# Kernel optimization log

Measured on AMD Instinct MI355X. Metric: run time of the kernel, lower is better.

The kernel has to match this reference:

```python
import jax, jax.numpy as jnp
import numpy as np

RHO = 1.0
L = 50
RS = np.array([20, 40, 80, 160], dtype=np.int32)

def _get_index():
    S = []
    for m in range(-L // 2, L // 2 + 1):
        for n in range(-L // 2, L // 2 + 1):
            if abs(m * n) <= RHO * L // 2:
                S.append((m, n))
    return np.array(S, dtype=np.int32)

IDX = _get_index()          # [449, 2] (m, n) pairs
K = IDX.shape[0]            # 449
B, N, M = 8, 65536, 2       # batch, sequence length, Nmodes (dual-pol)


def setup_inputs() -> dict:
    key = jax.random.key(0)
    ks = jax.random.split(key, 8)
    shp = (B, N, M)
    inp = {
        "E_real": jax.random.normal(ks[0], shp, jnp.float32),
        "E_imag": jax.random.normal(ks[1], shp, jnp.float32),
        "F_real": jax.random.normal(ks[2], shp, jnp.float32),
        "F_imag": jax.random.normal(ks[3], shp, jnp.float32),
        "C1_real": jax.random.normal(ks[4], (len(RS), K), jnp.float32) * 0.01,
        "C1_imag": jax.random.normal(ks[5], (len(RS), K), jnp.float32) * 0.01,
        "C2_real": jax.random.normal(ks[6], (len(RS), K), jnp.float32) * 0.01,
        "C2_imag": jax.random.normal(ks[7], (len(RS), K), jnp.float32) * 0.01,
    }
    # task_info columns: (P [dBm], Fi, Fs [Hz], Nch); Fs must be 2e9 * some Rs entry
    ti = np.zeros((B, 4), dtype=np.float32)
    ti[:, 0] = 2.0
    ti[:, 2] = RS[np.arange(B) % len(RS)].astype(np.float32) * 2e9
    inp["task_info"] = jnp.asarray(ti)
    return inp


def _forward(E_real, E_imag, F_real, F_imag, C1_real, C1_imag, C2_real, C2_imag, task_info):
    E = E_real + 1j * E_imag    # [B, N, M] complex64
    F = F_real + 1j * F_imag

    # choose_C: map Fs -> row of C tables (sorted-Rs order, as in the torch code)
    rs_sorted = jnp.sort(jnp.asarray(RS))
    x = (task_info[:, 2] / 2e9).astype(jnp.int32)              # [B]
    ind = jnp.argmax(x[:, None] == rs_sorted[None, :], axis=-1)  # [B]
    C1 = (C1_real + 1j * C1_imag)[ind]                         # [B, K]
    C2 = (C2_real + 1j * C2_imag)[ind]                         # [B, K]

    ms = jnp.asarray(IDX[:, 0])
    ns = jnp.asarray(IDX[:, 1])

    def step(acc, xs):
        m, n, c1, c2 = xs                                       # c1, c2: [B]
        En  = jnp.roll(E, n, axis=-2)
        Em  = jnp.roll(E, m, axis=-2)
        Emn = jnp.roll(E, m + n, axis=-2)
        Fn  = jnp.roll(F, n, axis=-2)
        Fmn = jnp.roll(F, m + n, axis=-2)
        A = En * jnp.conj(Fmn) * c1[:, None, None] + Fn * jnp.conj(Emn) * c2[:, None, None]
        # (A + A.roll(1, dim=-1)) swaps/combines the two polarizations
        return acc + (A + jnp.roll(A, 1, axis=-1)) * Em, None

    acc, _ = jax.lax.scan(step, jnp.zeros_like(E), (ms, ns, C1.T, C2.T))

    P = jnp.power(10.0, task_info[:, 0] / 10.0) / E.shape[-1]   # [B]
    Eo = F + (jnp.sqrt(P) ** 3)[:, None, None] * acc
    return E[:, L:-L, :], Eo[:, L:-L, :]


def reference(E_real, E_imag, F_real, F_imag, C1_real, C1_imag, C2_real, C2_imag, task_info):
    return _forward(E_real, E_imag, F_real, F_imag,
                    C1_real, C1_imag, C2_real, C2_imag, task_info)
```

## Files before the change

### kernel.cpp

```cpp
#include <hip/hip_runtime.h>
#include <hip/hip_bf16.h>


namespace {

constexpr int NSEQ    = 65536;
constexpr int BATCH   = 8;
constexpr int KTAPS   = 449;
constexpr int NM      = 25;
constexpr int THREADS = 256;
constexpr int TILE    = 512;
constexpr int WIN     = TILE + 4 * NM;
constexpr int GHW     = TILE + 2 * NM;

typedef float v2f __attribute__((ext_vector_type(2)));

__device__ inline v2f pkfma(float s, v2f v, v2f acc) {
  return __builtin_elementwise_fma((v2f){s, s}, v, acc);
}

__device__ inline unsigned short f2bf(float f) {
  __hip_bfloat16 h = __float2bfloat16(f);
  union { __hip_bfloat16 hh; unsigned short u; } cv;
  cv.hh = h;
  return cv.u;
}

__global__ void prep_c_kernel(const float* __restrict__ c1r, const float* __restrict__ c1i,
                              const float* __restrict__ c2r, const float* __restrict__ c2i,
                              float4* __restrict__ cw) {
  int idx = blockIdx.x * blockDim.x + threadIdx.x;
  if (idx < 4 * KTAPS) cw[idx] = make_float4(c1r[idx], c1i[idx], c2r[idx], c2i[idx]);
}

__device__ inline float4 gh_entry(const float4 e, const float4 f,
                                  const float4 fm, const float4 em) {
  v2f G = (v2f){fm.w * e.w, fm.w * (-e.z)};
  G = pkfma(fm.x, (v2f){e.x, e.y}, G);
  G = pkfma(fm.y, (v2f){e.y, -e.x}, G);
  G = pkfma(fm.z, (v2f){e.z, e.w}, G);
  v2f H = (v2f){em.w * f.w, em.w * (-f.z)};
  H = pkfma(em.x, (v2f){f.x, f.y}, H);
  H = pkfma(em.y, (v2f){f.y, -f.x}, H);
  H = pkfma(em.z, (v2f){f.z, f.w}, H);
  return make_float4(G.x, G.y, H.x, H.y);
}

__global__ __launch_bounds__(THREADS, 4) void hpbc_kernel(
    const float2* __restrict__ er, const float2* __restrict__ ei,
    const float2* __restrict__ fr, const float2* __restrict__ fi,
    const float*  __restrict__ task, const float4* __restrict__ cw,
    unsigned short* __restrict__ out, int nout, int lpad, int ntiles)
{
  __shared__ float4 sE[WIN];
  __shared__ float4 sF[WIN];
  __shared__ float4 sGH[2][GHW];

  const int bx   = blockIdx.x;
  const int b    = bx / ntiles;
  const int tile = bx - b * ntiles;
  const int tid  = threadIdx.x;
  const int i0   = lpad + tile * TILE;
  const int elo  = i0 - 2 * NM;

  const float2* erb = er + (size_t)b * NSEQ;
  const float2* eib = ei + (size_t)b * NSEQ;
  const float2* frb = fr + (size_t)b * NSEQ;
  const float2* fib = fi + (size_t)b * NSEQ;

  for (int u = tid; u < WIN; u += THREADS) {
    int g = (elo + u) & (NSEQ - 1);
    float2 a = erb[g], c = eib[g];
    sE[u] = make_float4(a.x, c.x, a.y, c.y);
    float2 d = frb[g], e = fib[g];
    sF[u] = make_float4(d.x, e.x, d.y, e.y);
  }

  const float dbm = task[b * 4 + 0];
  const float fsr = task[b * 4 + 2];
  const int   x   = (int)(fsr / 2.0e9f);
  const int ind = (x == 40) ? 1 : (x == 80) ? 2 : (x == 160) ? 3 : 0;
  const float4* __restrict__ crow = cw + ind * KTAPS;
  const float P  = powf(10.0f, dbm * 0.1f) * 0.5f;
  const float pf = P * sqrtf(P);

  __syncthreads();

  const float4 e0 = sE[tid + NM],            f0 = sF[tid + NM];
  const float4 e1 = sE[tid + THREADS + NM],  f1 = sF[tid + THREADS + NM];
  const bool  has3 = (tid < GHW - 2 * THREADS);
  float4 e2 = make_float4(0,0,0,0), f2 = e2;
  if (has3) { e2 = sE[tid + 2*THREADS + NM]; f2 = sF[tid + 2*THREADS + NM]; }

  v2f A0 = {0,0}, A1 = {0,0}, B0 = {0,0}, B1 = {0,0};
  int kbase = 0, p = 0;

  for (int mm = -NM; mm <= NM; ++mm) {
    {
      const int s = NM - mm;
      sGH[p][tid]             = gh_entry(e0, f0, sF[tid + s],             sE[tid + s]);
      sGH[p][tid + THREADS]   = gh_entry(e1, f1, sF[tid + THREADS + s],   sE[tid + THREADS + s]);
      if (has3)
        sGH[p][tid + 2*THREADS] = gh_entry(e2, f2, sF[tid + 2*THREADS + s], sE[tid + 2*THREADS + s]);
    }
    __syncthreads();

    const int am   = mm < 0 ? -mm : mm;
    const int nmax = (mm == 0) ? NM : (NM / am);
    const int T    = 2 * nmax + 1;
    const float4* __restrict__ gh = &sGH[p][0];
    const int base = 2 * tid + NM + nmax;
    v2f aU13={0,0}, aU42={0,0}, aV13={0,0}, aV42={0,0};
    v2f bU13={0,0}, bU42={0,0}, bV13={0,0}, bV42={0,0};
    float4 cp;
    {
      const float4 g = gh[base + 1];
      cp = crow[kbase];
      const v2f glo = (v2f){g.x, g.y}, ghi = (v2f){g.z, g.w};
      bU13 = pkfma(cp.x, glo, bU13); bU42 = pkfma(cp.y, glo, bU42);
      bV13 = pkfma(cp.z, ghi, bV13); bV42 = pkfma(cp.w, ghi, bV42);
    }
    for (int t = 1; t < T; ++t) {
      const float4 g = gh[base + 1 - t];
      const float4 c = crow[kbase + t];
      const v2f glo = (v2f){g.x, g.y}, ghi = (v2f){g.z, g.w};
      bU13 = pkfma(c.x,  glo, bU13); bU42 = pkfma(c.y,  glo, bU42);
      bV13 = pkfma(c.z,  ghi, bV13); bV42 = pkfma(c.w,  ghi, bV42);
      aU13 = pkfma(cp.x, glo, aU13); aU42 = pkfma(cp.y, glo, aU42);
      aV13 = pkfma(cp.z, ghi, aV13); aV42 = pkfma(cp.w, ghi, aV42);
      cp = c;
    }
    {
      const float4 g = gh[base + 1 - T];
      const v2f glo = (v2f){g.x, g.y}, ghi = (v2f){g.z, g.w};
      aU13 = pkfma(cp.x, glo, aU13); aU42 = pkfma(cp.y, glo, aU42);
      aV13 = pkfma(cp.z, ghi, aV13); aV42 = pkfma(cp.w, ghi, aV42);
    }
    kbase += T;

    const float sra = aU13.x - aU42.y + aV13.x - aV42.y;
    const float sia = aU13.y + aU42.x + aV13.y + aV42.x;
    const float srb = bU13.x - bU42.y + bV13.x - bV42.y;
    const float sib = bU13.y + bU42.x + bV13.y + bV42.x;

    const float4 ea = sE[2*tid + 2*NM - mm];
    const float4 eb = sE[2*tid + 1 + 2*NM - mm];
    A0 = pkfma(sra, (v2f){ea.x, ea.y}, pkfma(sia, (v2f){-ea.y, ea.x}, A0));
    A1 = pkfma(sra, (v2f){ea.z, ea.w}, pkfma(sia, (v2f){-ea.w, ea.z}, A1));
    B0 = pkfma(srb, (v2f){eb.x, eb.y}, pkfma(sib, (v2f){-eb.y, eb.x}, B0));
    B1 = pkfma(srb, (v2f){eb.z, eb.w}, pkfma(sib, (v2f){-eb.w, eb.z}, B1));
    p ^= 1;
  }

  const int end = lpad + nout;
  const size_t chunk1 = (size_t)BATCH * nout * 4;
  const int i = i0 + 2 * tid;
  if (i + 1 < end) {
    const float4 evA = sE[2*tid + 2*NM],     fvA = sF[2*tid + 2*NM];
    const float4 evB = sE[2*tid + 1 + 2*NM], fvB = sF[2*tid + 1 + 2*NM];
    const size_t o = ((size_t)b * nout + (size_t)(i - lpad)) * 4;
    ushort4 w0a, w0b, w1a, w1b;
    w0a.x = f2bf(evA.y); w0a.y = f2bf(evA.x); w0a.z = f2bf(evA.w); w0a.w = f2bf(evA.z);
    w0b.x = f2bf(evB.y); w0b.y = f2bf(evB.x); w0b.z = f2bf(evB.w); w0b.w = f2bf(evB.z);
    w1a.x = f2bf(fvA.y + pf * A0.y); w1a.y = f2bf(fvA.x + pf * A0.x);
    w1a.z = f2bf(fvA.w + pf * A1.y); w1a.w = f2bf(fvA.z + pf * A1.x);
    w1b.x = f2bf(fvB.y + pf * B0.y); w1b.y = f2bf(fvB.x + pf * B0.x);
    w1b.z = f2bf(fvB.w + pf * B1.y); w1b.w = f2bf(fvB.z + pf * B1.x);
    *reinterpret_cast<ushort4*>(out + o) = w0a;
    *reinterpret_cast<ushort4*>(out + o + 4) = w0b;
    *reinterpret_cast<ushort4*>(out + chunk1 + o) = w1a;
    *reinterpret_cast<ushort4*>(out + chunk1 + o + 4) = w1b;
  } else if (i < end) {
    const float4 evA = sE[2*tid + 2*NM], fvA = sF[2*tid + 2*NM];
    const size_t o = ((size_t)b * nout + (size_t)(i - lpad)) * 4;
    ushort4 w0a, w1a;
    w0a.x = f2bf(evA.y); w0a.y = f2bf(evA.x); w0a.z = f2bf(evA.w); w0a.w = f2bf(evA.z);
    w1a.x = f2bf(fvA.y + pf * A0.y); w1a.y = f2bf(fvA.x + pf * A0.x);
    w1a.z = f2bf(fvA.w + pf * A1.y); w1a.w = f2bf(fvA.z + pf * A1.x);
    *reinterpret_cast<ushort4*>(out + o) = w0a;
    *reinterpret_cast<ushort4*>(out + chunk1 + o) = w1a;
  }
}

}

extern "C" void kernel_launch(void* const* d_in, const int* in_sizes, int n_in,
                              void* d_out, int out_size, void* d_ws, size_t ws_size,
                              hipStream_t stream) {
  const float* E_real  = (const float*)d_in[0];
  const float* E_imag  = (const float*)d_in[1];
  const float* F_real  = (const float*)d_in[2];
  const float* F_imag  = (const float*)d_in[3];
  const float* C1_real = (const float*)d_in[4];
  const float* C1_imag = (const float*)d_in[5];
  const float* C2_real = (const float*)d_in[6];
  const float* C2_imag = (const float*)d_in[7];
  const float* task    = (const float*)d_in[8];

  int nout = out_size / 32;
  if (nout < 1 || nout > NSEQ) nout = NSEQ - 100;
  const int lpad   = (NSEQ - nout) / 2;
  const int ntiles = (nout + TILE - 1) / TILE;

  unsigned short* outp = (unsigned short*)d_out;
  float4* cw = (float4*)d_ws;

  hipLaunchKernelGGL(prep_c_kernel, dim3((4 * KTAPS + 255) / 256), dim3(256), 0, stream,
                     C1_real, C1_imag, C2_real, C2_imag, cw);

  hipLaunchKernelGGL(hpbc_kernel, dim3(BATCH * ntiles), dim3(THREADS), 0, stream,
                     (const float2*)E_real, (const float2*)E_imag,
                     (const float2*)F_real, (const float2*)F_imag,
                     task, cw, outp, nout, lpad, ntiles);
}
```

Baseline: 97.15 us.

## Split GH shared buffer into even/odd halves for conflict-free strided reads

```diff
diff --git a/kernel.cpp b/kernel.cpp
--- a/kernel.cpp
+++ b/kernel.cpp
@@ -12,11 +12,19 @@
 constexpr int TILE    = 512;
 constexpr int WIN     = TILE + 4 * NM;
 constexpr int GHW     = TILE + 2 * NM;
+constexpr int GHH     = (GHW + 1) / 2;
 
 typedef float v2f __attribute__((ext_vector_type(2)));
 
 __device__ inline v2f pkfma(float s, v2f v, v2f acc) {
   return __builtin_elementwise_fma((v2f){s, s}, v, acc);
+}
+
+__device__ inline void mac(v2f& U13, v2f& U42, v2f& V13, v2f& V42,
+                           const float4 c, const float4 g) {
+  const v2f glo = (v2f){g.x, g.y}, ghi = (v2f){g.z, g.w};
+  U13 = pkfma(c.x, glo, U13); U42 = pkfma(c.y, glo, U42);
+  V13 = pkfma(c.z, ghi, V13); V42 = pkfma(c.w, ghi, V42);
 }
 
 __device__ inline unsigned short f2bf(float f) {
@@ -54,7 +62,8 @@
 {
   __shared__ float4 sE[WIN];
   __shared__ float4 sF[WIN];
-  __shared__ float4 sGH[2][GHW];
+  __shared__ float4 ghE[2][GHH];
+  __shared__ float4 ghO[2][GHH];
 
   const int bx   = blockIdx.x;
   const int b    = bx / ntiles;
@@ -94,49 +103,58 @@
 
   v2f A0 = {0,0}, A1 = {0,0}, B0 = {0,0}, B1 = {0,0};
   int kbase = 0, p = 0;
+  float4 ebCarry = sE[2*tid + 1 + 2*NM + NM];
 
   for (int mm = -NM; mm <= NM; ++mm) {
     {
       const int s = NM - mm;
-      sGH[p][tid]             = gh_entry(e0, f0, sF[tid + s],             sE[tid + s]);
-      sGH[p][tid + THREADS]   = gh_entry(e1, f1, sF[tid + THREADS + s],   sE[tid + THREADS + s]);
-      if (has3)
-        sGH[p][tid + 2*THREADS] = gh_entry(e2, f2, sF[tid + 2*THREADS + s], sE[tid + 2*THREADS + s]);
+      const float4 g0 = gh_entry(e0, f0, sF[tid + s], sE[tid + s]);
+      if (tid & 1) ghO[p][tid >> 1] = g0; else ghE[p][tid >> 1] = g0;
+      const float4 g1 = gh_entry(e1, f1, sF[tid + THREADS + s], sE[tid + THREADS + s]);
+      if (tid & 1) ghO[p][(tid + THREADS) >> 1] = g1; else ghE[p][(tid + THREADS) >> 1] = g1;
+      if (has3) {
+        const float4 g2 = gh_entry(e2, f2, sF[tid + 2*THREADS + s], sE[tid + 2*THREADS + s]);
+        if (tid & 1) ghO[p][(tid + 2*THREADS) >> 1] = g2; else ghE[p][(tid + 2*THREADS) >> 1] = g2;
+      }
     }
     __syncthreads();
 
     const int am   = mm < 0 ? -mm : mm;
     const int nmax = (mm == 0) ? NM : (NM / am);
-    const int T    = 2 * nmax + 1;
-    const float4* __restrict__ gh = &sGH[p][0];
-    const int base = 2 * tid + NM + nmax;
+    const int q    = nmax & 1;
+    const float4* __restrict__ hiArr = q ? ghO[p] : ghE[p];
+    const float4* __restrict__ loArr = q ? ghE[p] : ghO[p];
+    const int h0 = tid + ((26 + nmax) >> 1);
+    const int h1 = tid + ((25 + nmax) >> 1);
+
     v2f aU13={0,0}, aU42={0,0}, aV13={0,0}, aV42={0,0};
     v2f bU13={0,0}, bU42={0,0}, bV13={0,0}, bV42={0,0};
-    float4 cp;
+    float4 cOdd;
     {
-      const float4 g = gh[base + 1];
-      cp = crow[kbase];
-      const v2f glo = (v2f){g.x, g.y}, ghi = (v2f){g.z, g.w};
-      bU13 = pkfma(cp.x, glo, bU13); bU42 = pkfma(cp.y, glo, bU42);
-      bV13 = pkfma(cp.z, ghi, bV13); bV42 = pkfma(cp.w, ghi, bV42);
-    }
-    for (int t = 1; t < T; ++t) {
-      const float4 g = gh[base + 1 - t];
-      const float4 c = crow[kbase + t];
-      const v2f glo = (v2f){g.x, g.y}, ghi = (v2f){g.z, g.w};
-      bU13 = pkfma(c.x,  glo, bU13); bU42 = pkfma(c.y,  glo, bU42);
-      bV13 = pkfma(c.z,  ghi, bV13); bV42 = pkfma(c.w,  ghi, bV42);
-      aU13 = pkfma(cp.x, glo, aU13); aU42 = pkfma(cp.y, glo, aU42);
-      aV13 = pkfma(cp.z, ghi, aV13); aV42 = pkfma(cp.w, ghi, aV42);
-      cp = c;
+      const float4 hi = hiArr[h0], lo = loArr[h1];
+      const float4 c0 = crow[kbase], c1 = crow[kbase + 1];
+      mac(bU13, bU42, bV13, bV42, c0, hi);
+      mac(bU13, bU42, bV13, bV42, c1, lo);
+      mac(aU13, aU42, aV13, aV42, c0, lo);
+      cOdd = c1;
+    }
+    for (int s = 1; s < nmax; ++s) {
+      const float4 hi = hiArr[h0 - s], lo = loArr[h1 - s];
+      const float4 c2 = crow[kbase + 2*s], c3 = crow[kbase + 2*s + 1];
+      mac(bU13, bU42, bV13, bV42, c2, hi);
+      mac(bU13, bU42, bV13, bV42, c3, lo);
+      mac(aU13, aU42, aV13, aV42, cOdd, hi);
+      mac(aU13, aU42, aV13, aV42, c2, lo);
+      cOdd = c3;
     }
     {
-      const float4 g = gh[base + 1 - T];
-      const v2f glo = (v2f){g.x, g.y}, ghi = (v2f){g.z, g.w};
-      aU13 = pkfma(cp.x, glo, aU13); aU42 = pkfma(cp.y, glo, aU42);
-      aV13 = pkfma(cp.z, ghi, aV13); aV42 = pkfma(cp.w, ghi, aV42);
-    }
-    kbase += T;
+      const float4 hi = hiArr[h0 - nmax], lo = loArr[h1 - nmax];
+      const float4 c2 = crow[kbase + 2*nmax];
+      mac(bU13, bU42, bV13, bV42, c2, hi);
+      mac(aU13, aU42, aV13, aV42, cOdd, hi);
+      mac(aU13, aU42, aV13, aV42, c2, lo);
+    }
+    kbase += 2 * nmax + 1;
 
     const float sra = aU13.x - aU42.y + aV13.x - aV42.y;
     const float sia = aU13.y + aU42.x + aV13.y + aV42.x;
@@ -144,7 +162,8 @@
     const float sib = bU13.y + bU42.x + bV13.y + bV42.x;
 
     const float4 ea = sE[2*tid + 2*NM - mm];
-    const float4 eb = sE[2*tid + 1 + 2*NM - mm];
+    const float4 eb = ebCarry;
+    ebCarry = ea;
     A0 = pkfma(sra, (v2f){ea.x, ea.y}, pkfma(sia, (v2f){-ea.y, ea.x}, A0));
     A1 = pkfma(sra, (v2f){ea.z, ea.w}, pkfma(sia, (v2f){-ea.w, ea.z}, A1));
     B0 = pkfma(srb, (v2f){eb.x, eb.y}, pkfma(sib, (v2f){-eb.y, eb.x}, B0));
```

After: 96.33 us. No clear change (-0.8%).

## Exploit ±m symmetry to share GH tables and compute four outputs per thread

Applied to the files above, without the earlier changes.

```diff
diff --git a/kernel.cpp b/kernel.cpp
--- a/kernel.cpp
+++ b/kernel.cpp
@@ -9,14 +9,23 @@
 constexpr int KTAPS   = 449;
 constexpr int NM      = 25;
 constexpr int THREADS = 256;
-constexpr int TILE    = 512;
+constexpr int TILE    = 1024;
 constexpr int WIN     = TILE + 4 * NM;
-constexpr int GHW     = TILE + 2 * NM;
+constexpr int WINQ    = WIN / 4;
+constexpr int GHW     = TILE + 2 * NM + 1;
+constexpr int GHH     = (GHW + 1) / 2;
 
 typedef float v2f __attribute__((ext_vector_type(2)));
 
 __device__ inline v2f pkfma(float s, v2f v, v2f acc) {
   return __builtin_elementwise_fma((v2f){s, s}, v, acc);
+}
+
+__device__ inline void mac(v2f& U13, v2f& U42, v2f& V13, v2f& V42,
+                           const float4 c, const float4 g) {
+  const v2f glo = (v2f){g.x, g.y}, ghi = (v2f){g.z, g.w};
+  U13 = pkfma(c.x, glo, U13); U42 = pkfma(c.y, glo, U42);
+  V13 = pkfma(c.z, ghi, V13); V42 = pkfma(c.w, ghi, V42);
 }
 
 __device__ inline unsigned short f2bf(float f) {
@@ -30,7 +39,10 @@
                               const float* __restrict__ c2r, const float* __restrict__ c2i,
                               float4* __restrict__ cw) {
   int idx = blockIdx.x * blockDim.x + threadIdx.x;
-  if (idx < 4 * KTAPS) cw[idx] = make_float4(c1r[idx], c1i[idx], c2r[idx], c2i[idx]);
+  if (idx < 4 * KTAPS) {
+    cw[idx]             = make_float4(c1r[idx], c1i[idx], c2r[idx], c2i[idx]);
+    cw[4 * KTAPS + idx] = make_float4(c2r[idx], c2i[idx], c1r[idx], c1i[idx]);
+  }
 }
 
 __device__ inline float4 gh_entry(const float4 e, const float4 f,
@@ -46,15 +58,48 @@
   return make_float4(G.x, G.y, H.x, H.y);
 }
 
-__global__ __launch_bounds__(THREADS, 4) void hpbc_kernel(
+template<int NMAX>
+__device__ inline void fir4(const float4* __restrict__ A0, const float4* __restrict__ A1,
+                            int b0, int b1, const float4* __restrict__ cc,
+                            v2f* __restrict__ acc )
+{
+  constexpr int T = 2 * NMAX + 1;
+  float4 cw0, cw1, cw2, cw3;
+#pragma unroll
+  for (int s = 0; s <= T + 2; ++s) {
+    const float4 g = (s & 1) ? A1[b1 - (s >> 1)] : A0[b0 - (s >> 1)];
+    if (s < T) cw0 = cc[s];
+    if (s <= T - 1)           mac(acc[12], acc[13], acc[14], acc[15], cw0, g);
+    if (s >= 1 && s <= T)     mac(acc[ 8], acc[ 9], acc[10], acc[11], cw1, g);
+    if (s >= 2 && s <= T + 1) mac(acc[ 4], acc[ 5], acc[ 6], acc[ 7], cw2, g);
+    if (s >= 3)               mac(acc[ 0], acc[ 1], acc[ 2], acc[ 3], cw3, g);
+    cw3 = cw2; cw2 = cw1; cw1 = cw0;
+  }
+}
+
+#define FIR_SWITCH(NMX, A0_, A1_, B0_, B1_, CC, ACC) \
+  switch (NMX) { \
+    case 25: fir4<25>(A0_, A1_, B0_, B1_, CC, ACC); break; \
+    case 12: fir4<12>(A0_, A1_, B0_, B1_, CC, ACC); break; \
+    case  8: fir4< 8>(A0_, A1_, B0_, B1_, CC, ACC); break; \
+    case  6: fir4< 6>(A0_, A1_, B0_, B1_, CC, ACC); break; \
+    case  5: fir4< 5>(A0_, A1_, B0_, B1_, CC, ACC); break; \
+    case  4: fir4< 4>(A0_, A1_, B0_, B1_, CC, ACC); break; \
+    case  3: fir4< 3>(A0_, A1_, B0_, B1_, CC, ACC); break; \
+    case  2: fir4< 2>(A0_, A1_, B0_, B1_, CC, ACC); break; \
+    default: fir4< 1>(A0_, A1_, B0_, B1_, CC, ACC); break; \
+  }
+
+__global__ __launch_bounds__(THREADS, 2) void hpbc_kernel(
     const float2* __restrict__ er, const float2* __restrict__ ei,
     const float2* __restrict__ fr, const float2* __restrict__ fi,
     const float*  __restrict__ task, const float4* __restrict__ cw,
     unsigned short* __restrict__ out, int nout, int lpad, int ntiles)
 {
-  __shared__ float4 sE[WIN];
+  __shared__ float4 sE4[4][WINQ];
   __shared__ float4 sF[WIN];
-  __shared__ float4 sGH[2][GHW];
+  __shared__ float4 ghE0[GHH], ghO0[GHH];
+  __shared__ float4 ghE1[GHH], ghO1[GHH];
 
   const int bx   = blockIdx.x;
   const int b    = bx / ntiles;
@@ -71,7 +116,7 @@
   for (int u = tid; u < WIN; u += THREADS) {
     int g = (elo + u) & (NSEQ - 1);
     float2 a = erb[g], c = eib[g];
-    sE[u] = make_float4(a.x, c.x, a.y, c.y);
+    sE4[u & 3][u >> 2] = make_float4(a.x, c.x, a.y, c.y);
     float2 d = frb[g], e = fib[g];
     sF[u] = make_float4(d.x, e.x, d.y, e.y);
   }
@@ -81,104 +126,123 @@
   const int   x   = (int)(fsr / 2.0e9f);
   const int ind = (x == 40) ? 1 : (x == 80) ? 2 : (x == 160) ? 3 : 0;
   const float4* __restrict__ crow = cw + ind * KTAPS;
+  const float4* __restrict__ cswp = cw + 4 * KTAPS + ind * KTAPS;
   const float P  = powf(10.0f, dbm * 0.1f) * 0.5f;
   const float pf = P * sqrtf(P);
 
   __syncthreads();
 
-  const float4 e0 = sE[tid + NM],            f0 = sF[tid + NM];
-  const float4 e1 = sE[tid + THREADS + NM],  f1 = sF[tid + THREADS + NM];
-  const bool  has3 = (tid < GHW - 2 * THREADS);
-  float4 e2 = make_float4(0,0,0,0), f2 = e2;
-  if (has3) { e2 = sE[tid + 2*THREADS + NM]; f2 = sF[tid + 2*THREADS + NM]; }
-
-  v2f A0 = {0,0}, A1 = {0,0}, B0 = {0,0}, B1 = {0,0};
-  int kbase = 0, p = 0;
-
-  for (int mm = -NM; mm <= NM; ++mm) {
+  const int pE = (tid + NM) & 3, iE = (tid + NM) >> 2;
+  float4 eH[5], fH[5];
+#pragma unroll
+  for (int k = 0; k < 4; ++k) { eH[k] = sE4[pE][iE + 64 * k]; fH[k] = sF[tid + NM + 256 * k]; }
+  const bool has5 = tid < GHW - 4 * THREADS;
+  if (has5) { eH[4] = sE4[pE][iE + 256]; fH[4] = sF[tid + NM + 1024]; }
+
+  auto write_gh = [&](float4* wE, float4* wO, int Mn) {
+    const int s  = NM - Mn;
+    const int pS = (tid + s) & 3, iS = (tid + s) >> 2;
+    const int wi = tid >> 1;
+#pragma unroll
+    for (int k = 0; k < 4; ++k) {
+      const float4 fm = sF[tid + s + 256 * k];
+      const float4 em = sE4[pS][iS + 64 * k];
+      const float4 gk = gh_entry(eH[k], fH[k], fm, em);
+      if (tid & 1) wO[wi + 128 * k] = gk; else wE[wi + 128 * k] = gk;
+    }
+    if (has5) {
+      const float4 fm = sF[tid + s + 1024];
+      const float4 em = sE4[pS][iS + 256];
+      const float4 gk = gh_entry(eH[4], fH[4], fm, em);
+      if (tid & 1) wO[wi + 512] = gk; else wE[wi + 512] = gk;
+    }
+  };
+
+  v2f O0[4], O1[4];
+#pragma unroll
+  for (int r = 0; r < 4; ++r) { O0[r] = (v2f){0, 0}; O1[r] = (v2f){0, 0}; }
+  int kbaseP = 199, kbaseN = 199;
+
+  auto iter = [&](const float4* rE, const float4* rO,
+                  float4* wE, float4* wO, int M) {
+    const int nmax = (M == 0) ? NM : (NM / M);
+    const int T    = 2 * nmax + 1;
+
     {
-      const int s = NM - mm;
-      sGH[p][tid]             = gh_entry(e0, f0, sF[tid + s],             sE[tid + s]);
-      sGH[p][tid + THREADS]   = gh_entry(e1, f1, sF[tid + THREADS + s],   sE[tid + THREADS + s]);
-      if (has3)
-        sGH[p][tid + 2*THREADS] = gh_entry(e2, f2, sF[tid + 2*THREADS + s], sE[tid + 2*THREADS + s]);
-    }
+      const int X = 28 + nmax;
+      const float4* A0 = (X & 1) ? rO : rE;
+      const float4* A1 = (X & 1) ? rE : rO;
+      const int b0 = 2 * tid + (X >> 1);
+      const int b1 = 2 * tid + ((X - 1) >> 1);
+      v2f acc[16];
+#pragma unroll
+      for (int j = 0; j < 16; ++j) acc[j] = (v2f){0, 0};
+      FIR_SWITCH(nmax, A0, A1, b0, b1, crow + kbaseP, acc);
+      kbaseP += T;
+#pragma unroll
+      for (int r = 0; r < 4; ++r) {
+        const float sr = acc[4*r].x - acc[4*r+1].y + acc[4*r+2].x - acc[4*r+3].y;
+        const float si = acc[4*r].y + acc[4*r+1].x + acc[4*r+2].y + acc[4*r+3].x;
+        const int u = 4 * tid + r + 2 * NM - M;
+        const float4 e = sE4[u & 3][u >> 2];
+        O0[r] = pkfma(sr, (v2f){e.x, e.y}, pkfma(si, (v2f){-e.y, e.x}, O0[r]));
+        O1[r] = pkfma(sr, (v2f){e.z, e.w}, pkfma(si, (v2f){-e.w, e.z}, O1[r]));
+      }
+    }
+
+    if (M > 0) {
+      kbaseN -= T;
+      const int X = 28 + nmax + M;
+      const float4* A0 = (X & 1) ? rO : rE;
+      const float4* A1 = (X & 1) ? rE : rO;
+      const int b0 = 2 * tid + (X >> 1);
+      const int b1 = 2 * tid + ((X - 1) >> 1);
+      v2f acc[16];
+#pragma unroll
+      for (int j = 0; j < 16; ++j) acc[j] = (v2f){0, 0};
+      FIR_SWITCH(nmax, A0, A1, b0, b1, cswp + kbaseN, acc);
+#pragma unroll
+      for (int r = 0; r < 4; ++r) {
+        const float sr = acc[4*r].x + acc[4*r+1].y + acc[4*r+2].x + acc[4*r+3].y;
+        const float si = acc[4*r+1].x - acc[4*r].y + acc[4*r+3].x - acc[4*r+2].y;
+        const int u = 4 * tid + r + 2 * NM + M;
+        const float4 e = sE4[u & 3][u >> 2];
+        O0[r] = pkfma(sr, (v2f){e.x, e.y}, pkfma(si, (v2f){-e.y, e.x}, O0[r]));
+        O1[r] = pkfma(sr, (v2f){e.z, e.w}, pkfma(si, (v2f){-e.w, e.z}, O1[r]));
+      }
+    }
+
+    if (M < NM) write_gh(wE, wO, M + 1);
     __syncthreads();
-
-    const int am   = mm < 0 ? -mm : mm;
-    const int nmax = (mm == 0) ? NM : (NM / am);
-    const int T    = 2 * nmax + 1;
-    const float4* __restrict__ gh = &sGH[p][0];
-    const int base = 2 * tid + NM + nmax;
-    v2f aU13={0,0}, aU42={0,0}, aV13={0,0}, aV42={0,0};
-    v2f bU13={0,0}, bU42={0,0}, bV13={0,0}, bV42={0,0};
-    float4 cp;
-    {
-      const float4 g = gh[base + 1];
-      cp = crow[kbase];
-      const v2f glo = (v2f){g.x, g.y}, ghi = (v2f){g.z, g.w};
-      bU13 = pkfma(cp.x, glo, bU13); bU42 = pkfma(cp.y, glo, bU42);
-      bV13 = pkfma(cp.z, ghi, bV13); bV42 = pkfma(cp.w, ghi, bV42);
-    }
-    for (int t = 1; t < T; ++t) {
-      const float4 g = gh[base + 1 - t];
-      const float4 c = crow[kbase + t];
-      const v2f glo = (v2f){g.x, g.y}, ghi = (v2f){g.z, g.w};
-      bU13 = pkfma(c.x,  glo, bU13); bU42 = pkfma(c.y,  glo, bU42);
-      bV13 = pkfma(c.z,  ghi, bV13); bV42 = pkfma(c.w,  ghi, bV42);
-      aU13 = pkfma(cp.x, glo, aU13); aU42 = pkfma(cp.y, glo, aU42);
-      aV13 = pkfma(cp.z, ghi, aV13); aV42 = pkfma(cp.w, ghi, aV42);
-      cp = c;
-    }
-    {
-      const float4 g = gh[base + 1 - T];
-      const v2f glo = (v2f){g.x, g.y}, ghi = (v2f){g.z, g.w};
-      aU13 = pkfma(cp.x, glo, aU13); aU42 = pkfma(cp.y, glo, aU42);
-      aV13 = pkfma(cp.z, ghi, aV13); aV42 = pkfma(cp.w, ghi, aV42);
-    }
-    kbase += T;
-
-    const float sra = aU13.x - aU42.y + aV13.x - aV42.y;
-    const float sia = aU13.y + aU42.x + aV13.y + aV42.x;
-    const float srb = bU13.x - bU42.y + bV13.x - bV42.y;
-    const float sib = bU13.y + bU42.x + bV13.y + bV42.x;
-
-    const float4 ea = sE[2*tid + 2*NM - mm];
-    const float4 eb = sE[2*tid + 1 + 2*NM - mm];
-    A0 = pkfma(sra, (v2f){ea.x, ea.y}, pkfma(sia, (v2f){-ea.y, ea.x}, A0));
-    A1 = pkfma(sra, (v2f){ea.z, ea.w}, pkfma(sia, (v2f){-ea.w, ea.z}, A1));
-    B0 = pkfma(srb, (v2f){eb.x, eb.y}, pkfma(sib, (v2f){-eb.y, eb.x}, B0));
-    B1 = pkfma(srb, (v2f){eb.z, eb.w}, pkfma(sib, (v2f){-eb.w, eb.z}, B1));
-    p ^= 1;
+  };
+
+  write_gh(ghE0, ghO0, 0);
+  __syncthreads();
+
+  for (int M = 0; M <= NM; M += 2) {
+    iter(ghE0, ghO0, ghE1, ghO1, M);
+    if (M + 1 <= NM)
+      iter(ghE1, ghO1, ghE0, ghO0, M + 1);
   }
 
   const int end = lpad + nout;
   const size_t chunk1 = (size_t)BATCH * nout * 4;
-  const int i = i0 + 2 * tid;
-  if (i + 1 < end) {
-    const float4 evA = sE[2*tid + 2*NM],     fvA = sF[2*tid + 2*NM];
-    const float4 evB = sE[2*tid + 1 + 2*NM], fvB = sF[2*tid + 1 + 2*NM];
-    const size_t o = ((size_t)b * nout + (size_t)(i - lpad)) * 4;
-    ushort4 w0a, w0b, w1a, w1b;
-    w0a.x = f2bf(evA.y); w0a.y = f2bf(evA.x); w0a.z = f2bf(evA.w); w0a.w = f2bf(evA.z);
-    w0b.x = f2bf(evB.y); w0b.y = f2bf(evB.x); w0b.z = f2bf(evB.w); w0b.w = f2bf(evB.z);
-    w1a.x = f2bf(fvA.y + pf * A0.y); w1a.y = f2bf(fvA.x + pf * A0.x);
-    w1a.z = f2bf(fvA.w + pf * A1.y); w1a.w = f2bf(fvA.z + pf * A1.x);
-    w1b.x = f2bf(fvB.y + pf * B0.y); w1b.y = f2bf(fvB.x + pf * B0.x);
-    w1b.z = f2bf(fvB.w + pf * B1.y); w1b.w = f2bf(fvB.z + pf * B1.x);
-    *reinterpret_cast<ushort4*>(out + o) = w0a;
-    *reinterpret_cast<ushort4*>(out + o + 4) = w0b;
-    *reinterpret_cast<ushort4*>(out + chunk1 + o) = w1a;
-    *reinterpret_cast<ushort4*>(out + chunk1 + o + 4) = w1b;
-  } else if (i < end) {
-    const float4 evA = sE[2*tid + 2*NM], fvA = sF[2*tid + 2*NM];
-    const size_t o = ((size_t)b * nout + (size_t)(i - lpad)) * 4;
-    ushort4 w0a, w1a;
-    w0a.x = f2bf(evA.y); w0a.y = f2bf(evA.x); w0a.z = f2bf(evA.w); w0a.w = f2bf(evA.z);
-    w1a.x = f2bf(fvA.y + pf * A0.y); w1a.y = f2bf(fvA.x + pf * A0.x);
-    w1a.z = f2bf(fvA.w + pf * A1.y); w1a.w = f2bf(fvA.z + pf * A1.x);
-    *reinterpret_cast<ushort4*>(out + o) = w0a;
-    *reinterpret_cast<ushort4*>(out + chunk1 + o) = w1a;
+#pragma unroll
+  for (int r = 0; r < 4; ++r) {
+    const int ii = 4 * tid + r;
+    const int i  = i0 + ii;
+    if (i < end) {
+      const int u = ii + 2 * NM;
+      const float4 ev = sE4[u & 3][u >> 2];
+      const float4 fv = sF[u];
+      const size_t o = ((size_t)b * nout + (size_t)(i - lpad)) * 4;
+      ushort4 w0, w1;
+      w0.x = f2bf(ev.y); w0.y = f2bf(ev.x); w0.z = f2bf(ev.w); w0.w = f2bf(ev.z);
+      w1.x = f2bf(fv.y + pf * O0[r].y); w1.y = f2bf(fv.x + pf * O0[r].x);
+      w1.z = f2bf(fv.w + pf * O1[r].y); w1.w = f2bf(fv.z + pf * O1[r].x);
+      *reinterpret_cast<ushort4*>(out + o) = w0;
+      *reinterpret_cast<ushort4*>(out + chunk1 + o) = w1;
+    }
   }
 }
 
```

Measured after the change: 82.97 us. -14.6%, faster.
